# Optimization experiments

Measured on AMD Instinct MI355X. Metric: run time of the kernel, lower is better.

Reference implementation:

```python
import jax, jax.numpy as jnp
import numpy as np

B, T, H, F = 64, 512, 512, 32
G = 4 * H  # PyTorch LSTM gate stack: i, f, g, o


def setup_inputs() -> dict:
    key = jax.random.key(0)
    ks = jax.random.split(key, 20)
    s = 1.0 / np.sqrt(H)  # PyTorch LSTM/Linear init scale

    def w(k, shape):
        return (jax.random.normal(k, shape, jnp.float32) * s).astype(jnp.float32)

    inp = {"x": jax.random.normal(ks[0], (B, T, F), jnp.float32)}
    shapes = {
        "enc_Wih0": (G, F), "enc_Whh0": (G, H), "enc_bih0": (G,), "enc_bhh0": (G,),
        "enc_Wih1": (G, H), "enc_Whh1": (G, H), "enc_bih1": (G,), "enc_bhh1": (G,),
        "dec_Wih0": (G, F), "dec_Whh0": (G, H), "dec_bih0": (G,), "dec_bhh0": (G,),
        "dec_Wih1": (G, H), "dec_Whh1": (G, H), "dec_bih1": (G,), "dec_bhh1": (G,),
        "W_out": (F, H), "b_out": (F,),
    }
    for i, (name, shp) in enumerate(shapes.items()):
        inp[name] = w(ks[i + 1], shp)
    return inp


def _cell(x, h, c, Wih, Whh, bih, bhh):
    gates = x @ Wih.T + h @ Whh.T + bih + bhh  # [B, 4H]
    i, f, g, o = jnp.split(gates, 4, axis=-1)
    c2 = jax.nn.sigmoid(f) * c + jax.nn.sigmoid(i) * jnp.tanh(g)
    h2 = jax.nn.sigmoid(o) * jnp.tanh(c2)
    return h2, c2


def _layer(xs, Wih, Whh, bih, bhh):
    # xs: [T, B, in]; zero initial state as in nn.LSTM default
    h0 = jnp.zeros((xs.shape[1], Whh.shape[1]), xs.dtype)

    def step(carry, xt):
        h, c = carry
        h2, c2 = _cell(xt, h, c, Wih, Whh, bih, bhh)
        return (h2, c2), h2

    (hT, cT), ys = jax.lax.scan(step, (h0, h0), xs)
    return ys, hT, cT


def _forward(x, eW0, eU0, eb0, ec0, eW1, eU1, eb1, ec1,
             dW0, dU0, db0, dc0, dW1, dU1, db1, dc1, Wo, bo):
    xs = jnp.transpose(x, (1, 0, 2))  # time-major [T, B, F]
    # 2-layer encoder (dropout=0 in eval-style deterministic reference)
    ys0, h0, c0 = _layer(xs, eW0, eU0, eb0, ec0)
    _, h1, c1 = _layer(ys0, eW1, eU1, eb1, ec1)

    # Decoder replays inputs in reversed time order (teacher forcing branch).
    # Output at step i uses dec_hidden[0][0,:] == layer-0 hidden BEFORE the step.
    def step(carry, xt):
        hA, cA, hB, cB = carry
        out = hA @ Wo.T + bo  # hidden2out on decoder layer-0 hidden (faithful to source)
        hA2, cA2 = _cell(xt, hA, cA, dW0, dU0, db0, dc0)
        hB2, cB2 = _cell(hA2, hB, cB, dW1, dU1, db1, dc1)
        return (hA2, cA2, hB2, cB2), out

    _, outs = jax.lax.scan(step, (h0, c0, h1, c1), xs[::-1])
    return jnp.transpose(outs[::-1], (1, 0, 2))  # back to [B, T, F]


def reference(x, enc_Wih0, enc_Whh0, enc_bih0, enc_bhh0, enc_Wih1, enc_Whh1, enc_bih1, enc_bhh1, dec_Wih0, dec_Whh0, dec_bih0, dec_bhh0, dec_Wih1, dec_Whh1, dec_bih1, dec_bhh1, W_out, b_out):
    return _forward(x, enc_Wih0, enc_Whh0, enc_bih0, enc_bhh0,
                    enc_Wih1, enc_Whh1, enc_bih1, enc_bhh1,
                    dec_Wih0, dec_Whh0, dec_bih0, dec_bhh0,
                    dec_Wih1, dec_Whh1, dec_bih1, dec_bhh1, W_out, b_out)
```

## Files before the change

### kernel.cpp

```cpp
#include <hip/hip_runtime.h>


#define BB   64
#define TT   512
#define HH   512
#define FF   32
#define KP   548
#define PODS 8
#define BT   8
#define GBLK 32
#define JT   16
#define NTHR 256
#define NBLK (PODS * GBLK)
#define GRS  66
#define GPL  (BT * GRS + 8)
#define GRF  (16 * GPL)
#define U_FLOATS  (BT * KP)
#define OP3F 32
#define LDS_FLOATS (U_FLOATS + 2 * GRF + 3 * OP3F)
#define LDS_BYTES  (LDS_FLOATS * 4)
#define PUB_U32  (2 * PODS * BT * HH)

typedef float f4v __attribute__((ext_vector_type(4)));
typedef float f2v __attribute__((ext_vector_type(2)));
typedef unsigned long long u64;
typedef unsigned int u32;

__device__ __forceinline__ float sigmf(float x)    { return 1.f / (1.f + __expf(-x)); }
__device__ __forceinline__ float tanhfast(float x) { return 1.f - 2.f / (__expf(2.f * x) + 1.f); }

__device__ __forceinline__ void load_w(
    const float* __restrict__ Wih, const float* __restrict__ Whh,
    const float* __restrict__ bih, const float* __restrict__ bhh,
    int j0, int w, int kap, int gt,
    f2v w01[4][8], f2v w23[4][8], f2v wxv[4], float bias[4])
{
  #pragma unroll
  for (int m = 0; m < 4; ++m) {
    const int g = m * HH + j0 + gt;
    #pragma unroll
    for (int q = 0; q < 8; ++q) {
      const f4v tw = *(const f4v*)&Whh[g * HH + w * 128 + q * 16 + kap * 4];
      f2v a; a[0] = tw[0]; a[1] = tw[1]; w01[m][q] = a;
      f2v b; b[0] = tw[2]; b[1] = tw[3]; w23[m][q] = b;
    }
    wxv[m]  = *(const f2v*)&Wih[g * FF + w * 8 + kap * 2];
    bias[m] = bih[g] + bhh[g];
  }
}

__global__ void init_ws_kernel(u32* pub) {
  const int i = blockIdx.x * blockDim.x + threadIdx.x;
  if (i < PUB_U32) pub[i] = 0u;
}

#define LDU64(P) __hip_atomic_load((P), __ATOMIC_RELAXED, __HIP_MEMORY_SCOPE_AGENT)

#define ISSUE(Q, GP) v[Q] = LDU64((const u64*)((GP) + 16 * (Q)))

#define WAITCH(Q) do {                                                         \
    unsigned lo_ = (unsigned)v[Q], hi_ = (unsigned)(v[Q] >> 32);               \
    int tries = 0;                                                             \
    while ((lo_ & 255u) != tg || (hi_ & 255u) != tg) {                         \
      if (++tries > 2) __builtin_amdgcn_s_sleep(1);                            \
      v[Q] = LDU64((const u64*)(gp + 16 * (Q)));                               \
      lo_ = (unsigned)v[Q]; hi_ = (unsigned)(v[Q] >> 32);                      \
    }                                                                          \
    float2 st_;                                                                \
    st_.x = __uint_as_float(lo_ & ~255u);                                      \
    st_.y = __uint_as_float(hi_ & ~255u);                                      \
    *(float2*)&Us[16 * (Q)] = st_;                                             \
  } while (0)

#define FMACHUNK(Q) do {                                                       \
    asm volatile("" ::: "memory");                                             \
    _Pragma("unroll")                                                          \
    for (int b = 0; b < 8; ++b) {                                              \
      const f4v u = *(const f4v*)&U[b * KP + w * 128 + 16 * (Q) + 4 * kap];    \
      f2v u01; u01[0] = u[0]; u01[1] = u[1];                                   \
      f2v u23; u23[0] = u[2]; u23[1] = u[3];                                   \
      _Pragma("unroll")                                                        \
      for (int m = 0; m < 4; ++m)                                              \
        acc2[m][b] += u01 * w01[m][Q] + u23 * w23[m][Q];                       \
    }                                                                          \
  } while (0)

__global__ void __launch_bounds__(NTHR, 1)
lstm_ae_kernel(const float* __restrict__ x,
               const float* __restrict__ eWih, const float* __restrict__ eWhh,
               const float* __restrict__ ebih, const float* __restrict__ ebhh,
               const float* __restrict__ dWih, const float* __restrict__ dWhh,
               const float* __restrict__ dbih, const float* __restrict__ dbhh,
               const float* __restrict__ Wo,  const float* __restrict__ bo,
               float* __restrict__ out, u32* __restrict__ pub)
{
  extern __shared__ float lds[];
  float* U   = lds;
  float* Gr  = lds + U_FLOATS;
  float* OP3 = lds + U_FLOATS + 2 * GRF;

  const int tid = threadIdx.x;
  const int blk = blockIdx.x;
  const int pod = blk & (PODS - 1);
  const int gb  = blk >> 3;
  const int b0  = pod * BT;
  const int j0  = gb * JT;

  const int w    = tid >> 6;
  const int lane = tid & 63;
  const int row  = lane >> 3;
  const int sub  = lane & 7;

  const int ks  = tid >> 4;
  const int kap = ks & 3;
  const int gt  = tid & 15;

  const bool upd = tid < BT * JT;
  const int  ub  = tid >> 4, ujl = tid & 15;
  float c_reg = 0.f;

  f2v   w01[4][8], w23[4][8], wxv[4];
  float bias[4];
  load_w(eWih, eWhh, ebih, ebhh, j0, w, kap, gt, w01, w23, wxv, bias);

  u64 v[8];
  {
    const u32* gp = pub + (size_t)pod * (BT * HH) + row * HH + 128 * w + 2 * sub;
    ISSUE(0, gp); ISSUE(1, gp); ISSUE(2, gp); ISSUE(3, gp);
  }

  #pragma unroll 1
  for (int phase = 0; phase < 2; ++phase) {
    #pragma unroll 1
    for (int step = 0; step < TT; ++step) {
      const int s = phase * TT + step;
      const unsigned tg = (unsigned)(s & 255);
      const int t = phase ? (TT - 1 - step) : step;
      const u32* prd = pub + (size_t)((s & 1) * PODS + pod) * (BT * HH);
      u32*       pwr = pub + (size_t)(((s + 1) & 1) * PODS + pod) * (BT * HH);
      float* Grp = Gr + (s & 1) * GRF;

      U[row * KP + HH + w * 8 + sub] =
          x[((size_t)(b0 + row) * TT + t) * FF + w * 8 + sub];

      float2 accinit; accinit.x = 0.f; accinit.y = 0.f;
      f2v acc2[4][8];
      #pragma unroll
      for (int m = 0; m < 4; ++m)
        #pragma unroll
        for (int b = 0; b < 8; ++b) {
          f2v z; z[0] = (ks == 0) ? bias[m] : 0.f; z[1] = 0.f;
          acc2[m][b] = z;
        }

      const u32* gp = prd + row * HH + 128 * w + 2 * sub;
      float*     Us = U + row * KP + 128 * w + 2 * sub;

      WAITCH(0); ISSUE(4, gp); FMACHUNK(0);
      WAITCH(1); ISSUE(5, gp); FMACHUNK(1);
      WAITCH(2); ISSUE(6, gp); FMACHUNK(2);
      WAITCH(3); ISSUE(7, gp); FMACHUNK(3);
      WAITCH(4); FMACHUNK(4);
      WAITCH(5); FMACHUNK(5);
      WAITCH(6); FMACHUNK(6);
      WAITCH(7); FMACHUNK(7);

      #pragma unroll
      for (int b = 0; b < 8; ++b) {
        const f2v ux = *(const f2v*)&U[b * KP + HH + w * 8 + 2 * kap];
        #pragma unroll
        for (int m = 0; m < 4; ++m)
          acc2[m][b] += ux * wxv[m];
      }
      {
        float* Gw = Grp + ks * GPL + gt;
        #pragma unroll
        for (int b = 0; b < 8; ++b)
          #pragma unroll
          for (int m = 0; m < 4; ++m)
            Gw[b * GRS + m * 16] = acc2[m][b][0] + acc2[m][b][1];
      }
      __syncthreads();

      if (upd) {
        const float* g0 = Grp + ub * GRS + ujl;
        float si = 0.f, sf = 0.f, sg = 0.f, so = 0.f;
        #pragma unroll
        for (int q = 0; q < 16; ++q) {
          const float* g = g0 + q * GPL;
          si += g[0]; sf += g[16]; sg += g[32]; so += g[48];
        }
        const float c2 = sigmf(sf) * c_reg + sigmf(si) * tanhfast(sg);
        const float h2 = sigmf(so) * tanhfast(c2);
        c_reg = c2;
        const unsigned pk = (__float_as_uint(h2) & ~255u)
                          | ((unsigned)(s + 1) & 255u);
        __hip_atomic_store(&pwr[ub * HH + j0 + ujl], pk,
                           __ATOMIC_RELAXED, __HIP_MEMORY_SCOPE_AGENT);
      }

      if (phase) {
        const float* wrow = Wo + gb * HH + w * 128 + sub * 16;
        const float* urow = U + row * KP + w * 128 + sub * 16;
        float pj = 0.f;
        #pragma unroll
        for (int k = 0; k < 16; k += 4) {
          const f4v wvv = *(const f4v*)(wrow + k);
          const f4v uvv = *(const f4v*)(urow + k);
          pj += uvv[0] * wvv[0] + uvv[1] * wvv[1] + uvv[2] * wvv[2] + uvv[3] * wvv[3];
        }
        pj += __shfl_xor(pj, 1);
        pj += __shfl_xor(pj, 2);
        pj += __shfl_xor(pj, 4);
        if (sub == 0) OP3[(s % 3) * OP3F + w * 8 + row] = pj;
        if (step > 0 && tid >= 192 && tid < 200) {
          const int b = tid - 192;
          const float* op = OP3 + ((s - 1) % 3) * OP3F + b;
          const float sm = op[0] + op[8] + op[16] + op[24];
          out[((size_t)(b0 + b) * TT + (t + 1)) * FF + gb] = sm + bo[gb];
        }
      }

      {
        const u32* gpn = (const u32*)pwr + row * HH + 128 * w + 2 * sub;
        ISSUE(0, gpn); ISSUE(1, gpn); ISSUE(2, gpn); ISSUE(3, gpn);
        asm volatile("" ::: "memory");
      }
    }
    if (phase == 0)
      load_w(dWih, dWhh, dbih, dbhh, j0, w, kap, gt, w01, w23, wxv, bias);
  }

  __syncthreads();
  if (tid >= 192 && tid < 200) {
    const int b = tid - 192;
    const float* op = OP3 + ((2 * TT - 1) % 3) * OP3F + b;
    const float sm = op[0] + op[8] + op[16] + op[24];
    out[((size_t)(b0 + b) * TT + 0) * FF + gb] = sm + bo[gb];
  }
}

extern "C" void kernel_launch(void* const* d_in, const int* in_sizes, int n_in,
                              void* d_out, int out_size, void* d_ws, size_t ws_size,
                              hipStream_t stream) {
  const float* x    = (const float*)d_in[0];
  const float* eWih = (const float*)d_in[1];
  const float* eWhh = (const float*)d_in[2];
  const float* ebih = (const float*)d_in[3];
  const float* ebhh = (const float*)d_in[4];
  const float* dWih = (const float*)d_in[9];
  const float* dWhh = (const float*)d_in[10];
  const float* dbih = (const float*)d_in[11];
  const float* dbhh = (const float*)d_in[12];
  const float* Wo   = (const float*)d_in[17];
  const float* bo   = (const float*)d_in[18];
  float* out = (float*)d_out;

  u32* pubbuf = (u32*)d_ws;

  hipFuncSetAttribute(reinterpret_cast<const void*>(lstm_ae_kernel),
                      hipFuncAttributeMaxDynamicSharedMemorySize, LDS_BYTES);

  init_ws_kernel<<<dim3((PUB_U32 + NTHR - 1) / NTHR), dim3(NTHR), 0, stream>>>(pubbuf);
  lstm_ae_kernel<<<dim3(NBLK), dim3(NTHR), LDS_BYTES, stream>>>(
      x, eWih, eWhh, ebih, ebhh, dWih, dWhh, dbih, dbhh, Wo, bo,
      out, pubbuf);
}
```

Baseline: 5.689 ms.

## Split each block's batch pod into two interleaved half-pods to hide sync latency

Each block now handles two independent 4-row batch groups and alternates between them every half-step. While one group waits on the cross-block hidden-state publish from its peers, the block computes the other group. The output projection is also restructured into a single full-wave reduction that writes directly, which drops the delayed OP3 ring buffer. The cost is twice as many barriers and spin-waits per timestep over smaller work units. The per-wave polling pattern also changes, now using four 64-bit loads per lane.

```diff
diff --git a/kernel.cpp b/kernel.cpp
--- a/kernel.cpp
+++ b/kernel.cpp
@@ -1,25 +1,16 @@
 #include <hip/hip_runtime.h>
 
 
-#define BB   64
 #define TT   512
 #define HH   512
 #define FF   32
 #define KP   548
-#define PODS 8
-#define BT   8
-#define GBLK 32
-#define JT   16
 #define NTHR 256
-#define NBLK (PODS * GBLK)
+#define NBLK 256
 #define GRS  66
-#define GPL  (BT * GRS + 8)
-#define GRF  (16 * GPL)
-#define U_FLOATS  (BT * KP)
-#define OP3F 32
-#define LDS_FLOATS (U_FLOATS + 2 * GRF + 3 * OP3F)
-#define LDS_BYTES  (LDS_FLOATS * 4)
-#define PUB_U32  (2 * PODS * BT * HH)
+#define GPL4 272
+#define GRF4 (16 * GPL4)
+#define PUB_U32 (2 * 16 * 4 * HH)
 
 typedef float f4v __attribute__((ext_vector_type(4)));
 typedef float f2v __attribute__((ext_vector_type(2)));
@@ -56,27 +47,25 @@
 
 #define LDU64(P) __hip_atomic_load((P), __ATOMIC_RELAXED, __HIP_MEMORY_SCOPE_AGENT)
 
-#define ISSUE(Q, GP) v[Q] = LDU64((const u64*)((GP) + 16 * (Q)))
-
 #define WAITCH(Q) do {                                                         \
     unsigned lo_ = (unsigned)v[Q], hi_ = (unsigned)(v[Q] >> 32);               \
     int tries = 0;                                                             \
     while ((lo_ & 255u) != tg || (hi_ & 255u) != tg) {                         \
       if (++tries > 2) __builtin_amdgcn_s_sleep(1);                            \
-      v[Q] = LDU64((const u64*)(gp + 16 * (Q)));                               \
+      v[Q] = LDU64((const u64*)(gp + 32 * (Q)));                               \
       lo_ = (unsigned)v[Q]; hi_ = (unsigned)(v[Q] >> 32);                      \
     }                                                                          \
     float2 st_;                                                                \
     st_.x = __uint_as_float(lo_ & ~255u);                                      \
     st_.y = __uint_as_float(hi_ & ~255u);                                      \
-    *(float2*)&Us[16 * (Q)] = st_;                                             \
+    *(float2*)&Us[32 * (Q)] = st_;                                             \
   } while (0)
 
 #define FMACHUNK(Q) do {                                                       \
     asm volatile("" ::: "memory");                                             \
     _Pragma("unroll")                                                          \
-    for (int b = 0; b < 8; ++b) {                                              \
-      const f4v u = *(const f4v*)&U[b * KP + w * 128 + 16 * (Q) + 4 * kap];    \
+    for (int b = 0; b < 4; ++b) {                                              \
+      const f4v u = *(const f4v*)&Up[b * KP + w * 128 + 16 * (Q) + 4 * kap];   \
       f2v u01; u01[0] = u[0]; u01[1] = u[1];                                   \
       f2v u23; u23[0] = u[2]; u23[1] = u[3];                                   \
       _Pragma("unroll")                                                        \
@@ -94,149 +83,147 @@
                const float* __restrict__ Wo,  const float* __restrict__ bo,
                float* __restrict__ out, u32* __restrict__ pub)
 {
-  extern __shared__ float lds[];
-  float* U   = lds;
-  float* Gr  = lds + U_FLOATS;
-  float* OP3 = lds + U_FLOATS + 2 * GRF;
+  __shared__ float UA[4 * KP];
+  __shared__ float UB[4 * KP];
+  __shared__ float Gr[2 * GRF4];
 
   const int tid = threadIdx.x;
   const int blk = blockIdx.x;
-  const int pod = blk & (PODS - 1);
+  const int pp  = blk & 7;
   const int gb  = blk >> 3;
-  const int b0  = pod * BT;
-  const int j0  = gb * JT;
+  const int j0  = gb * 16;
 
   const int w    = tid >> 6;
   const int lane = tid & 63;
-  const int row  = lane >> 3;
-  const int sub  = lane & 7;
+  const int grow = lane >> 4;
+  const int gsub = lane & 15;
 
   const int ks  = tid >> 4;
   const int kap = ks & 3;
   const int gt  = tid & 15;
 
-  const bool upd = tid < BT * JT;
-  const int  ub  = tid >> 4, ujl = tid & 15;
-  float c_reg = 0.f;
+  const int rb  = tid >> 4, rjl = tid & 15;
+  float cA = 0.f, cB = 0.f;
 
   f2v   w01[4][8], w23[4][8], wxv[4];
   float bias[4];
   load_w(eWih, eWhh, ebih, ebhh, j0, w, kap, gt, w01, w23, wxv, bias);
 
-  u64 v[8];
+  u64 v[4];
   {
-    const u32* gp = pub + (size_t)pod * (BT * HH) + row * HH + 128 * w + 2 * sub;
-    ISSUE(0, gp); ISSUE(1, gp); ISSUE(2, gp); ISSUE(3, gp);
+    const u32* gpn = pub + (size_t)pp * (4 * HH) + grow * HH + 128 * w + 2 * gsub;
+    v[0] = LDU64((const u64*)(gpn + 0));
+    v[1] = LDU64((const u64*)(gpn + 32));
+    v[2] = LDU64((const u64*)(gpn + 64));
+    v[3] = LDU64((const u64*)(gpn + 96));
   }
 
   #pragma unroll 1
-  for (int phase = 0; phase < 2; ++phase) {
-    #pragma unroll 1
-    for (int step = 0; step < TT; ++step) {
-      const int s = phase * TT + step;
-      const unsigned tg = (unsigned)(s & 255);
-      const int t = phase ? (TT - 1 - step) : step;
-      const u32* prd = pub + (size_t)((s & 1) * PODS + pod) * (BT * HH);
-      u32*       pwr = pub + (size_t)(((s + 1) & 1) * PODS + pod) * (BT * HH);
-      float* Grp = Gr + (s & 1) * GRF;
-
-      U[row * KP + HH + w * 8 + sub] =
-          x[((size_t)(b0 + row) * TT + t) * FF + w * 8 + sub];
-
-      float2 accinit; accinit.x = 0.f; accinit.y = 0.f;
-      f2v acc2[4][8];
+  for (int hi = 0; hi < 4 * TT; ++hi) {
+    if (hi == 2 * TT)
+      load_w(dWih, dWhh, dbih, dbhh, j0, w, kap, gt, w01, w23, wxv, bias);
+
+    const int sg     = hi >> 1;
+    const int podbit = hi & 1;
+    const int phase  = sg >> 9;
+    const int step   = sg & 511;
+    const int t      = phase ? (511 - step) : step;
+    const unsigned tg = (unsigned)(sg & 255);
+    const int podid  = pp + (podbit << 3);
+    const int b0     = podid * 4;
+    float* Up = podbit ? UB : UA;
+    const u32* prd = pub + (size_t)((sg & 1) * 16 + podid) * (4 * HH);
+    u32*       pwr = pub + (size_t)(((sg + 1) & 1) * 16 + podid) * (4 * HH);
+    float* Grp = Gr + (hi & 1) * GRF4;
+
+    if (lane < 32) {
+      const int xr = lane >> 3, xs = lane & 7;
+      Up[xr * KP + HH + 8 * w + xs] =
+          x[((size_t)(b0 + xr) * TT + t) * FF + 8 * w + xs];
+    }
+
+    f2v acc2[4][4];
+    #pragma unroll
+    for (int m = 0; m < 4; ++m)
+      #pragma unroll
+      for (int b = 0; b < 4; ++b) {
+        f2v z; z[0] = (ks == 0) ? bias[m] : 0.f; z[1] = 0.f;
+        acc2[m][b] = z;
+      }
+
+    const u32* gp = prd + grow * HH + 128 * w + 2 * gsub;
+    float*     Us = Up + grow * KP + 128 * w + 2 * gsub;
+    WAITCH(0); FMACHUNK(0); FMACHUNK(1);
+    WAITCH(1); FMACHUNK(2); FMACHUNK(3);
+    WAITCH(2); FMACHUNK(4); FMACHUNK(5);
+    WAITCH(3); FMACHUNK(6); FMACHUNK(7);
+
+    #pragma unroll
+    for (int b = 0; b < 4; ++b) {
+      const f2v ux = *(const f2v*)&Up[b * KP + HH + 8 * w + 2 * kap];
       #pragma unroll
       for (int m = 0; m < 4; ++m)
-        #pragma unroll
-        for (int b = 0; b < 8; ++b) {
-          f2v z; z[0] = (ks == 0) ? bias[m] : 0.f; z[1] = 0.f;
-          acc2[m][b] = z;
-        }
-
-      const u32* gp = prd + row * HH + 128 * w + 2 * sub;
-      float*     Us = U + row * KP + 128 * w + 2 * sub;
-
-      WAITCH(0); ISSUE(4, gp); FMACHUNK(0);
-      WAITCH(1); ISSUE(5, gp); FMACHUNK(1);
-      WAITCH(2); ISSUE(6, gp); FMACHUNK(2);
-      WAITCH(3); ISSUE(7, gp); FMACHUNK(3);
-      WAITCH(4); FMACHUNK(4);
-      WAITCH(5); FMACHUNK(5);
-      WAITCH(6); FMACHUNK(6);
-      WAITCH(7); FMACHUNK(7);
-
-      #pragma unroll
-      for (int b = 0; b < 8; ++b) {
-        const f2v ux = *(const f2v*)&U[b * KP + HH + w * 8 + 2 * kap];
+        acc2[m][b] += ux * wxv[m];
+    }
+    {
+      float* Gw = Grp + ks * GPL4 + gt;
+      #pragma unroll
+      for (int b = 0; b < 4; ++b)
         #pragma unroll
         for (int m = 0; m < 4; ++m)
-          acc2[m][b] += ux * wxv[m];
+          Gw[b * GRS + m * 16] = acc2[m][b][0] + acc2[m][b][1];
+    }
+    __syncthreads();
+
+    if (tid < 64) {
+      const float* g0 = Grp + rb * GRS + rjl;
+      float si = 0.f, sf = 0.f, sgg = 0.f, so = 0.f;
+      #pragma unroll
+      for (int q = 0; q < 16; ++q) {
+        const float* g = g0 + q * GPL4;
+        si += g[0]; sf += g[16]; sgg += g[32]; so += g[48];
       }
-      {
-        float* Gw = Grp + ks * GPL + gt;
-        #pragma unroll
-        for (int b = 0; b < 8; ++b)
-          #pragma unroll
-          for (int m = 0; m < 4; ++m)
-            Gw[b * GRS + m * 16] = acc2[m][b][0] + acc2[m][b][1];
-      }
-      __syncthreads();
-
-      if (upd) {
-        const float* g0 = Grp + ub * GRS + ujl;
-        float si = 0.f, sf = 0.f, sg = 0.f, so = 0.f;
-        #pragma unroll
-        for (int q = 0; q < 16; ++q) {
-          const float* g = g0 + q * GPL;
-          si += g[0]; sf += g[16]; sg += g[32]; so += g[48];
-        }
-        const float c2 = sigmf(sf) * c_reg + sigmf(si) * tanhfast(sg);
-        const float h2 = sigmf(so) * tanhfast(c2);
-        c_reg = c2;
-        const unsigned pk = (__float_as_uint(h2) & ~255u)
-                          | ((unsigned)(s + 1) & 255u);
-        __hip_atomic_store(&pwr[ub * HH + j0 + ujl], pk,
-                           __ATOMIC_RELAXED, __HIP_MEMORY_SCOPE_AGENT);
-      }
-
-      if (phase) {
-        const float* wrow = Wo + gb * HH + w * 128 + sub * 16;
-        const float* urow = U + row * KP + w * 128 + sub * 16;
-        float pj = 0.f;
-        #pragma unroll
-        for (int k = 0; k < 16; k += 4) {
-          const f4v wvv = *(const f4v*)(wrow + k);
-          const f4v uvv = *(const f4v*)(urow + k);
-          pj += uvv[0] * wvv[0] + uvv[1] * wvv[1] + uvv[2] * wvv[2] + uvv[3] * wvv[3];
-        }
-        pj += __shfl_xor(pj, 1);
-        pj += __shfl_xor(pj, 2);
-        pj += __shfl_xor(pj, 4);
-        if (sub == 0) OP3[(s % 3) * OP3F + w * 8 + row] = pj;
-        if (step > 0 && tid >= 192 && tid < 200) {
-          const int b = tid - 192;
-          const float* op = OP3 + ((s - 1) % 3) * OP3F + b;
-          const float sm = op[0] + op[8] + op[16] + op[24];
-          out[((size_t)(b0 + b) * TT + (t + 1)) * FF + gb] = sm + bo[gb];
-        }
-      }
-
-      {
-        const u32* gpn = (const u32*)pwr + row * HH + 128 * w + 2 * sub;
-        ISSUE(0, gpn); ISSUE(1, gpn); ISSUE(2, gpn); ISSUE(3, gpn);
-        asm volatile("" ::: "memory");
-      }
-    }
-    if (phase == 0)
-      load_w(dWih, dWhh, dbih, dbhh, j0, w, kap, gt, w01, w23, wxv, bias);
-  }
-
-  __syncthreads();
-  if (tid >= 192 && tid < 200) {
-    const int b = tid - 192;
-    const float* op = OP3 + ((2 * TT - 1) % 3) * OP3F + b;
-    const float sm = op[0] + op[8] + op[16] + op[24];
-    out[((size_t)(b0 + b) * TT + 0) * FF + gb] = sm + bo[gb];
+      const float c_old = podbit ? cB : cA;
+      const float c2 = sigmf(sf) * c_old + sigmf(si) * tanhfast(sgg);
+      const float h2 = sigmf(so) * tanhfast(c2);
+      if (podbit) cB = c2; else cA = c2;
+      const unsigned pk = (__float_as_uint(h2) & ~255u)
+                        | ((unsigned)(sg + 1) & 255u);
+      __hip_atomic_store(&pwr[rb * HH + j0 + rjl], pk,
+                         __ATOMIC_RELAXED, __HIP_MEMORY_SCOPE_AGENT);
+    }
+
+    if (phase) {
+      const float* Ur = Up + w * KP + lane * 8;
+      const float* Wr = Wo + gb * HH + lane * 8;
+      const f4v u0 = *(const f4v*)(Ur);
+      const f4v u1 = *(const f4v*)(Ur + 4);
+      const f4v q0 = *(const f4v*)(Wr);
+      const f4v q1 = *(const f4v*)(Wr + 4);
+      float pj = u0[0]*q0[0] + u0[1]*q0[1] + u0[2]*q0[2] + u0[3]*q0[3]
+               + u1[0]*q1[0] + u1[1]*q1[1] + u1[2]*q1[2] + u1[3]*q1[3];
+      pj += __shfl_xor(pj, 1);
+      pj += __shfl_xor(pj, 2);
+      pj += __shfl_xor(pj, 4);
+      pj += __shfl_xor(pj, 8);
+      pj += __shfl_xor(pj, 16);
+      pj += __shfl_xor(pj, 32);
+      if (lane == 0)
+        out[((size_t)(b0 + w) * TT + t) * FF + gb] = pj + bo[gb];
+    }
+
+    {
+      const int hin = hi + 1;
+      const int sgn = hin >> 1, pbn = hin & 1;
+      const int podn = pp + (pbn << 3);
+      const u32* gpn = pub + (size_t)((sgn & 1) * 16 + podn) * (4 * HH)
+                     + grow * HH + 128 * w + 2 * gsub;
+      v[0] = LDU64((const u64*)(gpn + 0));
+      v[1] = LDU64((const u64*)(gpn + 32));
+      v[2] = LDU64((const u64*)(gpn + 64));
+      v[3] = LDU64((const u64*)(gpn + 96));
+      asm volatile("" ::: "memory");
+    }
   }
 }
 
@@ -258,11 +245,8 @@
 
   u32* pubbuf = (u32*)d_ws;
 
-  hipFuncSetAttribute(reinterpret_cast<const void*>(lstm_ae_kernel),
-                      hipFuncAttributeMaxDynamicSharedMemorySize, LDS_BYTES);
-
   init_ws_kernel<<<dim3((PUB_U32 + NTHR - 1) / NTHR), dim3(NTHR), 0, stream>>>(pubbuf);
-  lstm_ae_kernel<<<dim3(NBLK), dim3(NTHR), LDS_BYTES, stream>>>(
+  lstm_ae_kernel<<<dim3(NBLK), dim3(NTHR), 0, stream>>>(
       x, eWih, eWhh, ebih, ebhh, dWih, dWhh, dbih, dbhh, Wo, bo,
       out, pubbuf);
 }
```

Measured after the change: 5.702 ms. Within noise of the previous version (+0.2%).

## Prefetch all eight hidden-state chunks early and vectorize gate partial-sum exchange

Applied to the files above, without the earlier changes.

Issues all eight polling loads for the next step's published hidden state right after the update store, instead of four after the output projection and four interleaved with the FMA chunks. The input-projection FMAs move ahead of the recurrent chunks. Gate partials are now stored and read as float4 per (j, gate) with a wider row stride, replacing scalar LDS traffic. This is meant to hide cross-block spin latency and cut LDS instructions, at the cost of more in-flight registers and earlier polling that may spin longer.

```diff
diff --git a/kernel.cpp b/kernel.cpp
--- a/kernel.cpp
+++ b/kernel.cpp
@@ -1,7 +1,6 @@
 #include <hip/hip_runtime.h>
 
 
-#define BB   64
 #define TT   512
 #define HH   512
 #define FF   32
@@ -12,7 +11,7 @@
 #define JT   16
 #define NTHR 256
 #define NBLK (PODS * GBLK)
-#define GRS  66
+#define GRS  68
 #define GPL  (BT * GRS + 8)
 #define GRF  (16 * GPL)
 #define U_FLOATS  (BT * KP)
@@ -125,8 +124,9 @@
 
   u64 v[8];
   {
-    const u32* gp = pub + (size_t)pod * (BT * HH) + row * HH + 128 * w + 2 * sub;
-    ISSUE(0, gp); ISSUE(1, gp); ISSUE(2, gp); ISSUE(3, gp);
+    const u32* gp0 = pub + (size_t)pod * (BT * HH) + row * HH + 128 * w + 2 * sub;
+    ISSUE(0, gp0); ISSUE(1, gp0); ISSUE(2, gp0); ISSUE(3, gp0);
+    ISSUE(4, gp0); ISSUE(5, gp0); ISSUE(6, gp0); ISSUE(7, gp0);
   }
 
   #pragma unroll 1
@@ -143,7 +143,6 @@
       U[row * KP + HH + w * 8 + sub] =
           x[((size_t)(b0 + row) * TT + t) * FF + w * 8 + sub];
 
-      float2 accinit; accinit.x = 0.f; accinit.y = 0.f;
       f2v acc2[4][8];
       #pragma unroll
       for (int m = 0; m < 4; ++m)
@@ -153,42 +152,44 @@
           acc2[m][b] = z;
         }
 
+      #pragma unroll
+      for (int b = 0; b < 8; ++b) {
+        const f2v ux = *(const f2v*)&U[b * KP + HH + w * 8 + 2 * kap];
+        #pragma unroll
+        for (int m = 0; m < 4; ++m)
+          acc2[m][b] += ux * wxv[m];
+      }
+
       const u32* gp = prd + row * HH + 128 * w + 2 * sub;
       float*     Us = U + row * KP + 128 * w + 2 * sub;
-
-      WAITCH(0); ISSUE(4, gp); FMACHUNK(0);
-      WAITCH(1); ISSUE(5, gp); FMACHUNK(1);
-      WAITCH(2); ISSUE(6, gp); FMACHUNK(2);
-      WAITCH(3); ISSUE(7, gp); FMACHUNK(3);
+      WAITCH(0); FMACHUNK(0);
+      WAITCH(1); FMACHUNK(1);
+      WAITCH(2); FMACHUNK(2);
+      WAITCH(3); FMACHUNK(3);
       WAITCH(4); FMACHUNK(4);
       WAITCH(5); FMACHUNK(5);
       WAITCH(6); FMACHUNK(6);
       WAITCH(7); FMACHUNK(7);
 
-      #pragma unroll
-      for (int b = 0; b < 8; ++b) {
-        const f2v ux = *(const f2v*)&U[b * KP + HH + w * 8 + 2 * kap];
-        #pragma unroll
-        for (int m = 0; m < 4; ++m)
-          acc2[m][b] += ux * wxv[m];
-      }
       {
-        float* Gw = Grp + ks * GPL + gt;
-        #pragma unroll
-        for (int b = 0; b < 8; ++b)
+        float* Gw = Grp + ks * GPL + gt * 4;
+        #pragma unroll
+        for (int b = 0; b < 8; ++b) {
+          f4v r;
           #pragma unroll
-          for (int m = 0; m < 4; ++m)
-            Gw[b * GRS + m * 16] = acc2[m][b][0] + acc2[m][b][1];
+          for (int m = 0; m < 4; ++m) r[m] = acc2[m][b][0] + acc2[m][b][1];
+          *(f4v*)&Gw[b * GRS] = r;
+        }
       }
       __syncthreads();
 
       if (upd) {
-        const float* g0 = Grp + ub * GRS + ujl;
+        const float* g0 = Grp + ub * GRS + ujl * 4;
         float si = 0.f, sf = 0.f, sg = 0.f, so = 0.f;
         #pragma unroll
         for (int q = 0; q < 16; ++q) {
-          const float* g = g0 + q * GPL;
-          si += g[0]; sf += g[16]; sg += g[32]; so += g[48];
+          const f4v g = *(const f4v*)(g0 + q * GPL);
+          si += g[0]; sf += g[1]; sg += g[2]; so += g[3];
         }
         const float c2 = sigmf(sf) * c_reg + sigmf(si) * tanhfast(sg);
         const float h2 = sigmf(so) * tanhfast(c2);
@@ -197,6 +198,13 @@
                           | ((unsigned)(s + 1) & 255u);
         __hip_atomic_store(&pwr[ub * HH + j0 + ujl], pk,
                            __ATOMIC_RELAXED, __HIP_MEMORY_SCOPE_AGENT);
+      }
+
+      {
+        const u32* gpn = (const u32*)pwr + row * HH + 128 * w + 2 * sub;
+        ISSUE(0, gpn); ISSUE(1, gpn); ISSUE(2, gpn); ISSUE(3, gpn);
+        ISSUE(4, gpn); ISSUE(5, gpn); ISSUE(6, gpn); ISSUE(7, gpn);
+        asm volatile("" ::: "memory");
       }
 
       if (phase) {
@@ -219,12 +227,6 @@
           const float sm = op[0] + op[8] + op[16] + op[24];
           out[((size_t)(b0 + b) * TT + (t + 1)) * FF + gb] = sm + bo[gb];
         }
-      }
-
-      {
-        const u32* gpn = (const u32*)pwr + row * HH + 128 * w + 2 * sub;
-        ISSUE(0, gpn); ISSUE(1, gpn); ISSUE(2, gpn); ISSUE(3, gpn);
-        asm volatile("" ::: "memory");
       }
     }
     if (phase == 0)
```

New measurement: 6.583 ms. 1.16x slower.
